# Kernel optimization log

Measured on AMD Instinct MI355X. Metric: run time of the kernel, lower is better.

The kernel has to match this reference:

```python
import jax, jax.numpy as jnp
import numpy as np

D_MODEL = 1024
N_HEADS = 16
HEAD_DIM = D_MODEL // N_HEADS


def setup_inputs() -> dict:
    key = jax.random.key(0)
    k_x, k_qkv, k_out = jax.random.split(key, 3)
    B, T = 4, 2048
    x = jax.random.normal(k_x, (B, T, D_MODEL), dtype=jnp.float32)
    # Linear(bias=False): y = x @ W, with W stored as [in, out]
    W_qkv = jax.random.normal(k_qkv, (D_MODEL, 3 * D_MODEL), dtype=jnp.float32) * (D_MODEL ** -0.5)
    W_out = jax.random.normal(k_out, (D_MODEL, D_MODEL), dtype=jnp.float32) * (D_MODEL ** -0.5)
    return {"x": x, "W_qkv": W_qkv, "W_out": W_out}


def reference(x, W_qkv, W_out):
    B, T, C = x.shape
    H, Dh = N_HEADS, HEAD_DIM
    scale = 1.0 / jnp.sqrt(jnp.asarray(Dh, dtype=x.dtype))

    qkv = x @ W_qkv  # [B,T,3C]
    q, k, v = jnp.split(qkv, 3, axis=-1)

    def split_heads(t):
        return t.reshape(B, T, H, Dh).transpose(0, 2, 1, 3)  # [B,H,T,Dh]

    q, k, v = split_heads(q), split_heads(k), split_heads(v)

    scores = jnp.einsum('bhqd,bhkd->bhqk', q, k) * scale  # [B,H,T,T]
    causal = jnp.tril(jnp.ones((T, T), dtype=bool))
    scores = jnp.where(causal, scores, jnp.asarray(-jnp.inf, dtype=scores.dtype))
    attn = jax.nn.softmax(scores, axis=-1)
    # dropout p=0.0 -> identity
    out = jnp.einsum('bhqk,bhkd->bhqd', attn, v)  # [B,H,T,Dh]
    out = out.transpose(0, 2, 1, 3).reshape(B, T, C)
    return out @ W_out
```

## Files before the change

### kernel.cpp

```cpp
#include <hip/hip_runtime.h>
#include <stdint.h>

typedef unsigned short u16;
typedef float f32x4 __attribute__((ext_vector_type(4)));
typedef short s16x8 __attribute__((ext_vector_type(8)));

#define SEQ 2048
#define DM 1024
#define NH 16
#define HD 64
#define BATCH 4
#define ROWS (BATCH*SEQ)

__device__ __forceinline__ u16 f32_bf16(float f) {
  union { float f; uint32_t u; } c; c.f = f;
  uint32_t u = c.u;
  return (u16)((u + 0x7fffu + ((u >> 16) & 1u)) >> 16);
}
__device__ __forceinline__ u16 f32_bf16_trunc(float f) {
  union { float f; uint32_t u; } c; c.f = f;
  return (u16)(c.u >> 16);
}

#define GLOAD_LDS16(g, l) __builtin_amdgcn_global_load_lds( \
    (__attribute__((address_space(1))) void*)(g),           \
    (__attribute__((address_space(3))) void*)(l), 16, 0, 0)

__global__ __launch_bounds__(256) void cast_bf16_k(const float* __restrict__ in,
                                                   u16* __restrict__ out, int n4) {
  int i = blockIdx.x * 256 + threadIdx.x;
  if (i >= n4) return;
  float4 v = ((const float4*)in)[i];
  ushort4 o;
  o.x = f32_bf16(v.x); o.y = f32_bf16(v.y); o.z = f32_bf16(v.z); o.w = f32_bf16(v.w);
  ((ushort4*)out)[i] = o;
}

__global__ __launch_bounds__(256) void cast_transpose_k(const float* __restrict__ in,
                                                        u16* __restrict__ out, int R, int C) {
  __shared__ float tile[32][33];
  int c0 = blockIdx.x * 32, r0 = blockIdx.y * 32;
  int t = threadIdx.x;
  int lr = t >> 3, lc = (t & 7) * 4;
  float4 v = *(const float4*)(in + (size_t)(r0 + lr) * C + c0 + lc);
  tile[lr][lc] = v.x; tile[lr][lc + 1] = v.y; tile[lr][lc + 2] = v.z; tile[lr][lc + 3] = v.w;
  __syncthreads();
  ushort4 o;
  o.x = f32_bf16(tile[lc + 0][lr]);
  o.y = f32_bf16(tile[lc + 1][lr]);
  o.z = f32_bf16(tile[lc + 2][lr]);
  o.w = f32_bf16(tile[lc + 3][lr]);
  *(ushort4*)(out + (size_t)(c0 + lr) * R + r0 + lc) = o;
}

#define QSCALE 0.18033688011112042f


__device__ __forceinline__ f32x4 mfma16(s16x8 a, s16x8 b, f32x4 c) {
  return __builtin_amdgcn_mfma_f32_16x16x32_bf16(a, b, c, 0, 0, 0);
}

template<int STG, int ENDVM, int LAST>
__device__ __forceinline__ void tile_step(
    const u16* lAc, const u16* lBc,
    const u16* lAn, const u16* lBn,
    u16* lAs, u16* lBs,
    const u16* gA0, const u16* gA1, const u16* gB0, const u16* gB1,
    int d0, int d1, int aoff, int boff,
    s16x8 (&fa)[4], s16x8 (&fb)[4],
    s16x8 (&na)[4], s16x8 (&nb)[4],
    f32x4 (&acc)[8][4])
{
  __builtin_amdgcn_s_barrier();
  __builtin_amdgcn_sched_barrier(0);
  s16x8 f1[4];
#pragma unroll
  for (int mi = 0; mi < 4; ++mi) f1[mi] = *(const s16x8*)&lAc[aoff + 2048 + mi * 512];
  if (STG) { GLOAD_LDS16(gA0, lAs + d0); GLOAD_LDS16(gA1, lAs + d1); }
  asm volatile("s_waitcnt lgkmcnt(4)" ::: "memory");
  __builtin_amdgcn_sched_barrier(0);
  __builtin_amdgcn_s_setprio(1);
#pragma unroll
  for (int mi = 0; mi < 4; ++mi)
#pragma unroll
    for (int ni = 0; ni < 4; ++ni)
      acc[mi][ni] = mfma16(fa[mi], fb[ni], acc[mi][ni]);
  __builtin_amdgcn_s_setprio(0);
  __builtin_amdgcn_sched_barrier(0);
  if (STG) { GLOAD_LDS16(gB0, lBs + d0); GLOAD_LDS16(gB1, lBs + d1); }
  if (ENDVM == 8)      asm volatile("s_waitcnt vmcnt(8)" ::: "memory");
  else if (ENDVM == 4) asm volatile("s_waitcnt vmcnt(4)" ::: "memory");
  else if (ENDVM == 0) asm volatile("s_waitcnt vmcnt(0)" ::: "memory");
  __builtin_amdgcn_s_barrier();
  __builtin_amdgcn_sched_barrier(0);
  if (!LAST) {
#pragma unroll
    for (int ni = 0; ni < 4; ++ni) nb[ni] = *(const s16x8*)&lBn[boff + ni * 512];
#pragma unroll
    for (int mi = 0; mi < 4; ++mi) na[mi] = *(const s16x8*)&lAn[aoff + mi * 512];
    asm volatile("s_waitcnt lgkmcnt(8)" ::: "memory");
  } else {
    asm volatile("s_waitcnt lgkmcnt(0)" ::: "memory");
  }
  __builtin_amdgcn_sched_barrier(0);
  __builtin_amdgcn_s_setprio(1);
#pragma unroll
  for (int mi = 0; mi < 4; ++mi)
#pragma unroll
    for (int ni = 0; ni < 4; ++ni)
      acc[4 + mi][ni] = mfma16(f1[mi], fb[ni], acc[4 + mi][ni]);
  __builtin_amdgcn_s_setprio(0);
  __builtin_amdgcn_sched_barrier(0);
}

__global__ __launch_bounds__(512, 2) void qkv_gemm(
    const u16* __restrict__ A, const u16* __restrict__ Bt,
    u16* __restrict__ Qo, u16* __restrict__ Ko, u16* __restrict__ Vo)
{
  __shared__ u16 lA[4][8192];
  __shared__ u16 lB[4][8192];
  int t = threadIdx.x;

  int flat = blockIdx.y * 12 + blockIdx.x;
  int xcd = flat & 7, idx = flat >> 3;
  int by = (xcd >> 1) * 8 + idx / 6;
  int bx = (xcd & 1) * 6 + idx % 6;
  int m0 = by * 256, n0 = bx * 256;

  int lane = t & 63, w = t >> 6;
  int m16 = lane & 15, quad = lane >> 4;
  int wm = w >> 2, wn = w & 3;

  int r0 = t >> 2;
  int scol = ((t & 3) ^ ((t >> 3) & 3)) * 8;
  const u16* Ag0 = A  + (size_t)(m0 + r0) * DM + scol;
  const u16* Ag1 = A  + (size_t)(m0 + 128 + r0) * DM + scol;
  const u16* Bg0 = Bt + (size_t)(n0 + r0) * DM + scol;
  const u16* Bg1 = Bt + (size_t)(n0 + 128 + r0) * DM + scol;
  int d0 = t * 8, d1 = 4096 + t * 8;

  int ka = (quad ^ ((m16 >> 1) & 3)) * 8;
  int aoff = (wm * 128 + m16) * 32 + ka;
  int boff = (wn * 64 + m16) * 32 + ka;

  f32x4 acc[8][4];
#pragma unroll
  for (int mi = 0; mi < 8; ++mi)
#pragma unroll
    for (int ni = 0; ni < 4; ++ni)
#pragma unroll
      for (int r = 0; r < 4; ++r) acc[mi][ni][r] = 0.f;

#pragma unroll
  for (int kt = 0; kt < 3; ++kt) {
    GLOAD_LDS16(Ag0 + kt * 32, lA[kt] + d0);
    GLOAD_LDS16(Ag1 + kt * 32, lA[kt] + d1);
    GLOAD_LDS16(Bg0 + kt * 32, lB[kt] + d0);
    GLOAD_LDS16(Bg1 + kt * 32, lB[kt] + d1);
  }
  asm volatile("s_waitcnt vmcnt(8)" ::: "memory");
  __builtin_amdgcn_s_barrier();
  __builtin_amdgcn_sched_barrier(0);

  s16x8 fa0[4], fb0[4], fa1[4], fb1[4];
#pragma unroll
  for (int ni = 0; ni < 4; ++ni) fb0[ni] = *(const s16x8*)&lB[0][boff + ni * 512];
#pragma unroll
  for (int mi = 0; mi < 4; ++mi) fa0[mi] = *(const s16x8*)&lA[0][aoff + mi * 512];

  for (int it = 0; it < 14; ++it) {
    int T = 2 * it;
    tile_step<1, 8, 0>(lA[T & 3], lB[T & 3], lA[(T + 1) & 3], lB[(T + 1) & 3],
                       lA[(T + 3) & 3], lB[(T + 3) & 3],
                       Ag0 + (T + 3) * 32, Ag1 + (T + 3) * 32,
                       Bg0 + (T + 3) * 32, Bg1 + (T + 3) * 32,
                       d0, d1, aoff, boff, fa0, fb0, fa1, fb1, acc);
    tile_step<1, 8, 0>(lA[(T + 1) & 3], lB[(T + 1) & 3], lA[(T + 2) & 3], lB[(T + 2) & 3],
                       lA[(T + 4) & 3], lB[(T + 4) & 3],
                       Ag0 + (T + 4) * 32, Ag1 + (T + 4) * 32,
                       Bg0 + (T + 4) * 32, Bg1 + (T + 4) * 32,
                       d0, d1, aoff, boff, fa1, fb1, fa0, fb0, acc);
  }
  tile_step<1, 8, 0>(lA[0], lB[0], lA[1], lB[1], lA[3], lB[3],
                     Ag0 + 31 * 32, Ag1 + 31 * 32, Bg0 + 31 * 32, Bg1 + 31 * 32,
                     d0, d1, aoff, boff, fa0, fb0, fa1, fb1, acc);
  tile_step<0, 4, 0>(lA[1], lB[1], lA[2], lB[2], lA[0], lB[0],
                     Ag0, Ag1, Bg0, Bg1, d0, d1, aoff, boff, fa1, fb1, fa0, fb0, acc);
  tile_step<0, 0, 0>(lA[2], lB[2], lA[3], lB[3], lA[0], lB[0],
                     Ag0, Ag1, Bg0, Bg1, d0, d1, aoff, boff, fa0, fb0, fa1, fb1, acc);
  tile_step<0, -1, 1>(lA[3], lB[3], lA[0], lB[0], lA[0], lB[0],
                      Ag0, Ag1, Bg0, Bg1, d0, d1, aoff, boff, fa1, fb1, fa0, fb0, acc);

#pragma unroll
  for (int mi = 0; mi < 8; ++mi) {
    int gr = m0 + wm * 128 + mi * 16 + quad * 4;
    int b = gr >> 11, tt = gr & 2047;
#pragma unroll
    for (int ni = 0; ni < 4; ++ni) {
      int gc = n0 + wn * 64 + ni * 16 + m16;
      int sec = gc >> 10, rem = gc & 1023, h = rem >> 6, d = rem & 63;
      if (sec == 0) {
#pragma unroll
        for (int r = 0; r < 4; ++r)
          Qo[(((size_t)b * NH + h) * SEQ + tt + r) * HD + d] = f32_bf16(acc[mi][ni][r] * QSCALE);
      } else if (sec == 1) {
#pragma unroll
        for (int r = 0; r < 4; ++r)
          Ko[(((size_t)b * NH + h) * SEQ + tt + r) * HD + d] = f32_bf16(acc[mi][ni][r]);
      } else {
        ushort4 o;
        o.x = f32_bf16(acc[mi][ni][0]); o.y = f32_bf16(acc[mi][ni][1]);
        o.z = f32_bf16(acc[mi][ni][2]); o.w = f32_bf16(acc[mi][ni][3]);
        *(ushort4*)&Vo[(((size_t)b * NH + h) * HD + d) * SEQ + tt] = o;
      }
    }
  }
}

template<int EPI>
__global__ __launch_bounds__(256) void gemm_bt(
    const u16* __restrict__ A, const u16* __restrict__ Bt,
    float* __restrict__ Cf, u16* __restrict__ Qo, u16* __restrict__ Ko, u16* __restrict__ Vo,
    int M, int N, int K)
{
  __shared__ u16 As[128 * 32];
  __shared__ u16 Bs[128 * 32];
  int t = threadIdx.x;
  int m0 = blockIdx.y * 128, n0 = blockIdx.x * 128;

  int srow = t >> 2, scol8 = (t & 3) * 8;
  const u16* Ag0 = A  + (size_t)(m0 + srow) * K + scol8;
  const u16* Ag1 = A  + (size_t)(m0 + 64 + srow) * K + scol8;
  const u16* Bg0 = Bt + (size_t)(n0 + srow) * K + scol8;
  const u16* Bg1 = Bt + (size_t)(n0 + 64 + srow) * K + scol8;
  u16* Al0 = As + t * 8;  u16* Al1 = As + 2048 + t * 8;
  u16* Bl0 = Bs + t * 8;  u16* Bl1 = Bs + 2048 + t * 8;

  int lane = t & 63, w = t >> 6;
  int m16 = lane & 15, quad = lane >> 4;
  int wr = (w >> 1) * 64, wc = (w & 1) * 64;

  f32x4 acc[4][4];
#pragma unroll
  for (int mi = 0; mi < 4; ++mi)
#pragma unroll
    for (int ni = 0; ni < 4; ++ni)
#pragma unroll
      for (int r = 0; r < 4; ++r) acc[mi][ni][r] = 0.f;

  for (int k0 = 0; k0 < K; k0 += 32) {
    __syncthreads();
    GLOAD_LDS16(Ag0 + k0, Al0);
    GLOAD_LDS16(Ag1 + k0, Al1);
    GLOAD_LDS16(Bg0 + k0, Bl0);
    GLOAD_LDS16(Bg1 + k0, Bl1);
    __syncthreads();
    s16x8 af[4], bf[4];
#pragma unroll
    for (int mi = 0; mi < 4; ++mi)
      af[mi] = *(const s16x8*)(As + (wr + mi * 16 + m16) * 32 + quad * 8);
#pragma unroll
    for (int ni = 0; ni < 4; ++ni)
      bf[ni] = *(const s16x8*)(Bs + (wc + ni * 16 + m16) * 32 + quad * 8);
#pragma unroll
    for (int mi = 0; mi < 4; ++mi)
#pragma unroll
      for (int ni = 0; ni < 4; ++ni)
        acc[mi][ni] = __builtin_amdgcn_mfma_f32_16x16x32_bf16(af[mi], bf[ni], acc[mi][ni], 0, 0, 0);
  }

  if (EPI == 0) {
#pragma unroll
    for (int mi = 0; mi < 4; ++mi) {
      int gr = m0 + wr + mi * 16 + quad * 4;
#pragma unroll
      for (int ni = 0; ni < 4; ++ni) {
        int gc = n0 + wc + ni * 16 + m16;
#pragma unroll
        for (int r = 0; r < 4; ++r)
          Cf[(size_t)(gr + r) * N + gc] = acc[mi][ni][r];
      }
    }
  } else {
#pragma unroll
    for (int mi = 0; mi < 4; ++mi) {
      int gr = m0 + wr + mi * 16 + quad * 4;
      int b = gr >> 11, tt = gr & 2047;
#pragma unroll
      for (int ni = 0; ni < 4; ++ni) {
        int gc = n0 + wc + ni * 16 + m16;
        int sec = gc >> 10, rem = gc & 1023, h = rem >> 6, d = rem & 63;
        if (sec == 0) {
#pragma unroll
          for (int r = 0; r < 4; ++r)
            Qo[(((size_t)b * NH + h) * SEQ + tt + r) * HD + d] = f32_bf16(acc[mi][ni][r] * QSCALE);
        } else if (sec == 1) {
#pragma unroll
          for (int r = 0; r < 4; ++r)
            Ko[(((size_t)b * NH + h) * SEQ + tt + r) * HD + d] = f32_bf16(acc[mi][ni][r]);
        } else {
          ushort4 o;
          o.x = f32_bf16(acc[mi][ni][0]); o.y = f32_bf16(acc[mi][ni][1]);
          o.z = f32_bf16(acc[mi][ni][2]); o.w = f32_bf16(acc[mi][ni][3]);
          *(ushort4*)&Vo[(((size_t)b * NH + h) * HD + d) * SEQ + tt] = o;
        }
      }
    }
  }
}

__global__ __launch_bounds__(256) void attn_k(
    const u16* __restrict__ Q, const u16* __restrict__ K,
    const u16* __restrict__ Vt_g,
    u16* __restrict__ O)
{
  __shared__ u16 Ks[64][72];
  __shared__ u16 Vt[64][72];
  __shared__ u16 Ps[4][32][72];
  int flat = blockIdx.y * 8 + blockIdx.x;
  int xcd = flat & 7, pos = flat >> 3;
  int bh = xcd * 8 + (pos >> 3);
  int xb = pos & 7;
  int t = threadIdx.x, w = t >> 6, lane = t & 63;
  int m16 = lane & 15, quad = lane >> 4;
  int b = bh >> 4, h = bh & 15;

  int srow = t >> 2, sc = (t & 3) * 16;
  const u16* Kg0 = K    + ((size_t)bh * SEQ + srow) * HD  + sc;
  const u16* Vg0 = Vt_g + ((size_t)bh * HD  + srow) * SEQ + sc;

  for (int half = 0; half < 2; ++half) {
    int qt = half ? (15 - xb) : xb;
    int q0 = qt * 128;

    const u16* QbA = Q + ((size_t)bh * SEQ + q0 + w * 32 + m16) * HD + quad * 8;
    s16x8 qA0 = *(const s16x8*)QbA;
    s16x8 qA1 = *(const s16x8*)(QbA + 32);
    s16x8 qB0 = *(const s16x8*)(QbA + 16 * HD);
    s16x8 qB1 = *(const s16x8*)(QbA + 16 * HD + 32);

    f32x4 accA[4], accB[4];
    float lA = 0.f, lB = 0.f;
#pragma unroll
    for (int ni = 0; ni < 4; ++ni)
#pragma unroll
      for (int r = 0; r < 4; ++r) { accA[ni][r] = 0.f; accB[ni][r] = 0.f; }

    int ktmax = 2 * qt + 1;
    for (int kt = 0; kt <= ktmax; ++kt) {
      uint4 kv0 = *(const uint4*)(Kg0 + (size_t)kt * 64 * HD);
      uint4 kv1 = *(const uint4*)(Kg0 + (size_t)kt * 64 * HD + 8);
      uint4 vv0 = *(const uint4*)(Vg0 + kt * 64);
      uint4 vv1 = *(const uint4*)(Vg0 + kt * 64 + 8);
      __syncthreads();
      *(uint4*)&Ks[srow][sc]     = kv0;
      *(uint4*)&Ks[srow][sc + 8] = kv1;
      *(uint4*)&Vt[srow][sc]     = vv0;
      *(uint4*)&Vt[srow][sc + 8] = vv1;
      __syncthreads();

      f32x4 sA[4], sB[4];
#pragma unroll
      for (int ni = 0; ni < 4; ++ni)
#pragma unroll
        for (int r = 0; r < 4; ++r) { sA[ni][r] = 0.f; sB[ni][r] = 0.f; }
#pragma unroll
      for (int ni = 0; ni < 4; ++ni) {
        s16x8 kf0 = *(const s16x8*)&Ks[ni * 16 + m16][quad * 8];
        s16x8 kf1 = *(const s16x8*)&Ks[ni * 16 + m16][32 + quad * 8];
        sA[ni] = mfma16(kf0, qA0, sA[ni]);
        sA[ni] = mfma16(kf1, qA1, sA[ni]);
        sB[ni] = mfma16(kf0, qB0, sB[ni]);
        sB[ni] = mfma16(kf1, qB1, sB[ni]);
      }
      if (kt >= 2 * qt) {
        int qga = q0 + w * 32 + m16;
#pragma unroll
        for (int ni = 0; ni < 4; ++ni) {
          int kb = kt * 64 + ni * 16 + quad * 4;
#pragma unroll
          for (int r = 0; r < 4; ++r) {
            if (kb + r > qga)      sA[ni][r] = -1e30f;
            if (kb + r > qga + 16) sB[ni][r] = -1e30f;
          }
        }
      }

#pragma unroll
      for (int ni = 0; ni < 4; ++ni) {
        ushort4 oA, oB;
#pragma unroll
        for (int r = 0; r < 4; ++r) {
          float pA = __builtin_amdgcn_exp2f(sA[ni][r]);
          float pB = __builtin_amdgcn_exp2f(sB[ni][r]);
          lA += pA; lB += pB;
          ((u16*)&oA)[r] = f32_bf16_trunc(pA);
          ((u16*)&oB)[r] = f32_bf16_trunc(pB);
        }
        *(ushort4*)&Ps[w][m16][ni * 16 + quad * 4]      = oA;
        *(ushort4*)&Ps[w][16 + m16][ni * 16 + quad * 4] = oB;
      }

#pragma unroll
      for (int ks = 0; ks < 2; ++ks) {
        s16x8 pA = *(const s16x8*)&Ps[w][m16][ks * 32 + quad * 8];
        s16x8 pB = *(const s16x8*)&Ps[w][16 + m16][ks * 32 + quad * 8];
#pragma unroll
        for (int ni = 0; ni < 4; ++ni) {
          s16x8 vf = *(const s16x8*)&Vt[ni * 16 + m16][ks * 32 + quad * 8];
          accA[ni] = mfma16(pA, vf, accA[ni]);
          accB[ni] = mfma16(pB, vf, accB[ni]);
        }
      }
    }

    lA += __shfl_xor(lA, 16, 64);
    lA += __shfl_xor(lA, 32, 64);
    lB += __shfl_xor(lB, 16, 64);
    lB += __shfl_xor(lB, 32, 64);

#pragma unroll
    for (int r = 0; r < 4; ++r) {
      int src = (lane & 48) | (quad * 4 + r);
      float la = __shfl(lA, src, 64);
      float lb = __shfl(lB, src, 64);
      float ia = 1.f / la, ib = 1.f / lb;
      int qa = q0 + w * 32 + quad * 4 + r;
      size_t baseA = ((size_t)(b * SEQ + qa)) * DM + h * HD;
      size_t baseB = baseA + (size_t)16 * DM;
#pragma unroll
      for (int ni = 0; ni < 4; ++ni) {
        O[baseA + ni * 16 + m16] = f32_bf16(accA[ni][r] * ia);
        O[baseB + ni * 16 + m16] = f32_bf16(accB[ni][r] * ib);
      }
    }
  }
}

extern "C" void kernel_launch(void* const* d_in, const int* in_sizes, int n_in,
                              void* d_out, int out_size, void* d_ws, size_t ws_size,
                              hipStream_t stream) {
  const float* x    = (const float*)d_in[0];
  const float* Wqkv = (const float*)d_in[1];
  const float* Wout = (const float*)d_in[2];
  float* out = (float*)d_out;

  u16* ws = (u16*)d_ws;
  size_t off = 0;
  u16* x_bf   = ws + off; off += (size_t)ROWS * DM;
  u16* wqkv_t = ws + off; off += (size_t)(3 * DM) * DM;
  u16* wout_t = ws + off; off += (size_t)DM * DM;
  u16* Qb     = ws + off; off += (size_t)BATCH * NH * SEQ * HD;
  u16* Kb     = ws + off; off += (size_t)BATCH * NH * SEQ * HD;
  u16* Vb     = ws + off; off += (size_t)BATCH * NH * SEQ * HD;
  u16* AO     = ws + off; off += (size_t)ROWS * DM;

  cast_bf16_k<<<(ROWS * DM / 4 + 255) / 256, 256, 0, stream>>>(x, x_bf, ROWS * DM / 4);
  cast_transpose_k<<<dim3(3 * DM / 32, DM / 32), 256, 0, stream>>>(Wqkv, wqkv_t, DM, 3 * DM);
  cast_transpose_k<<<dim3(DM / 32, DM / 32), 256, 0, stream>>>(Wout, wout_t, DM, DM);
  qkv_gemm<<<dim3(12, 32), 512, 0, stream>>>(x_bf, wqkv_t, Qb, Kb, Vb);
  attn_k<<<dim3(8, BATCH * NH), 256, 0, stream>>>(Qb, Kb, Vb, AO);
  gemm_bt<0><<<dim3(DM / 128, ROWS / 128), 256, 0, stream>>>(
      AO, wout_t, out, nullptr, nullptr, nullptr, ROWS, DM, DM);
}
```

Before: 255.7 us.

## Restructure QKV GEMM pipeline into double-buffered 64-wide K tiles

Replaces the four-stage 32-wide K ring buffer with cross-step fragment prefetch by a two-buffer scheme where each step covers 64 K elements in four sub-phases. Fragments are loaded and consumed within the same sub-phase, with barriers around each load and a full lgkmcnt wait. The goal is simpler scheduling with fewer register-held fragments and larger loads per stage. The cost is less LDS-read/MFMA overlap and more barriers per K tile, so latency may be exposed.

```diff
diff --git a/kernel.cpp b/kernel.cpp
--- a/kernel.cpp
+++ b/kernel.cpp
@@ -60,65 +60,90 @@
   return __builtin_amdgcn_mfma_f32_16x16x32_bf16(a, b, c, 0, 0, 0);
 }
 
-template<int STG, int ENDVM, int LAST>
-__device__ __forceinline__ void tile_step(
-    const u16* lAc, const u16* lBc,
-    const u16* lAn, const u16* lBn,
-    u16* lAs, u16* lBs,
+template<int STG, int VM2, int VM4>
+__device__ __forceinline__ void qkv_tile(
+    const u16* Ac, const u16* Bc,
+    u16* Asd, u16* Bsd,
     const u16* gA0, const u16* gA1, const u16* gB0, const u16* gB1,
     int d0, int d1, int aoff, int boff,
-    s16x8 (&fa)[4], s16x8 (&fb)[4],
-    s16x8 (&na)[4], s16x8 (&nb)[4],
     f32x4 (&acc)[8][4])
 {
-  __builtin_amdgcn_s_barrier();
-  __builtin_amdgcn_sched_barrier(0);
-  s16x8 f1[4];
-#pragma unroll
-  for (int mi = 0; mi < 4; ++mi) f1[mi] = *(const s16x8*)&lAc[aoff + 2048 + mi * 512];
-  if (STG) { GLOAD_LDS16(gA0, lAs + d0); GLOAD_LDS16(gA1, lAs + d1); }
-  asm volatile("s_waitcnt lgkmcnt(4)" ::: "memory");
+  s16x8 bfr[4], af[4];
+#pragma unroll
+  for (int ni = 0; ni < 4; ++ni) bfr[ni] = *(const s16x8*)&Bc[boff + ni * 512];
+#pragma unroll
+  for (int mi = 0; mi < 4; ++mi) af[mi] = *(const s16x8*)&Ac[aoff + mi * 512];
+  if (STG) { GLOAD_LDS16(gA0, Asd + d0); GLOAD_LDS16(gA1, Asd + d1); }
+  __builtin_amdgcn_s_barrier();
+  asm volatile("s_waitcnt lgkmcnt(0)" ::: "memory");
   __builtin_amdgcn_sched_barrier(0);
   __builtin_amdgcn_s_setprio(1);
 #pragma unroll
   for (int mi = 0; mi < 4; ++mi)
 #pragma unroll
     for (int ni = 0; ni < 4; ++ni)
-      acc[mi][ni] = mfma16(fa[mi], fb[ni], acc[mi][ni]);
+      acc[mi][ni] = mfma16(af[mi], bfr[ni], acc[mi][ni]);
   __builtin_amdgcn_s_setprio(0);
   __builtin_amdgcn_sched_barrier(0);
-  if (STG) { GLOAD_LDS16(gB0, lBs + d0); GLOAD_LDS16(gB1, lBs + d1); }
-  if (ENDVM == 8)      asm volatile("s_waitcnt vmcnt(8)" ::: "memory");
-  else if (ENDVM == 4) asm volatile("s_waitcnt vmcnt(4)" ::: "memory");
-  else if (ENDVM == 0) asm volatile("s_waitcnt vmcnt(0)" ::: "memory");
-  __builtin_amdgcn_s_barrier();
-  __builtin_amdgcn_sched_barrier(0);
-  if (!LAST) {
-#pragma unroll
-    for (int ni = 0; ni < 4; ++ni) nb[ni] = *(const s16x8*)&lBn[boff + ni * 512];
-#pragma unroll
-    for (int mi = 0; mi < 4; ++mi) na[mi] = *(const s16x8*)&lAn[aoff + mi * 512];
-    asm volatile("s_waitcnt lgkmcnt(8)" ::: "memory");
-  } else {
-    asm volatile("s_waitcnt lgkmcnt(0)" ::: "memory");
-  }
+  __builtin_amdgcn_s_barrier();
+#pragma unroll
+  for (int mi = 0; mi < 4; ++mi) af[mi] = *(const s16x8*)&Ac[aoff + 2048 + mi * 512];
+  if (STG) { GLOAD_LDS16(gB0, Bsd + d0); GLOAD_LDS16(gB1, Bsd + d1); }
+  __builtin_amdgcn_s_barrier();
+  asm volatile("s_waitcnt lgkmcnt(0)" ::: "memory");
   __builtin_amdgcn_sched_barrier(0);
   __builtin_amdgcn_s_setprio(1);
 #pragma unroll
   for (int mi = 0; mi < 4; ++mi)
 #pragma unroll
     for (int ni = 0; ni < 4; ++ni)
-      acc[4 + mi][ni] = mfma16(f1[mi], fb[ni], acc[4 + mi][ni]);
+      acc[4 + mi][ni] = mfma16(af[mi], bfr[ni], acc[4 + mi][ni]);
   __builtin_amdgcn_s_setprio(0);
   __builtin_amdgcn_sched_barrier(0);
+  if (VM2 == 4)      asm volatile("s_waitcnt vmcnt(4)" ::: "memory");
+  else if (VM2 == 0) asm volatile("s_waitcnt vmcnt(0)" ::: "memory");
+  __builtin_amdgcn_s_barrier();
+#pragma unroll
+  for (int ni = 0; ni < 4; ++ni) bfr[ni] = *(const s16x8*)&Bc[8192 + boff + ni * 512];
+#pragma unroll
+  for (int mi = 0; mi < 4; ++mi) af[mi] = *(const s16x8*)&Ac[8192 + aoff + mi * 512];
+  if (STG) { GLOAD_LDS16(gA0 + 32, Asd + 8192 + d0); GLOAD_LDS16(gA1 + 32, Asd + 8192 + d1); }
+  __builtin_amdgcn_s_barrier();
+  asm volatile("s_waitcnt lgkmcnt(0)" ::: "memory");
+  __builtin_amdgcn_sched_barrier(0);
+  __builtin_amdgcn_s_setprio(1);
+#pragma unroll
+  for (int mi = 0; mi < 4; ++mi)
+#pragma unroll
+    for (int ni = 0; ni < 4; ++ni)
+      acc[mi][ni] = mfma16(af[mi], bfr[ni], acc[mi][ni]);
+  __builtin_amdgcn_s_setprio(0);
+  __builtin_amdgcn_sched_barrier(0);
+  __builtin_amdgcn_s_barrier();
+#pragma unroll
+  for (int mi = 0; mi < 4; ++mi) af[mi] = *(const s16x8*)&Ac[8192 + aoff + 2048 + mi * 512];
+  if (STG) { GLOAD_LDS16(gB0 + 32, Bsd + 8192 + d0); GLOAD_LDS16(gB1 + 32, Bsd + 8192 + d1); }
+  __builtin_amdgcn_s_barrier();
+  asm volatile("s_waitcnt lgkmcnt(0)" ::: "memory");
+  __builtin_amdgcn_sched_barrier(0);
+  __builtin_amdgcn_s_setprio(1);
+#pragma unroll
+  for (int mi = 0; mi < 4; ++mi)
+#pragma unroll
+    for (int ni = 0; ni < 4; ++ni)
+      acc[4 + mi][ni] = mfma16(af[mi], bfr[ni], acc[4 + mi][ni]);
+  __builtin_amdgcn_s_setprio(0);
+  __builtin_amdgcn_sched_barrier(0);
+  if (VM4 == 4) asm volatile("s_waitcnt vmcnt(4)" ::: "memory");
+  __builtin_amdgcn_s_barrier();
 }
 
 __global__ __launch_bounds__(512, 2) void qkv_gemm(
     const u16* __restrict__ A, const u16* __restrict__ Bt,
     u16* __restrict__ Qo, u16* __restrict__ Ko, u16* __restrict__ Vo)
 {
-  __shared__ u16 lA[4][8192];
-  __shared__ u16 lB[4][8192];
+  __shared__ u16 lA[2][16384];
+  __shared__ u16 lB[2][16384];
   int t = threadIdx.x;
 
   int flat = blockIdx.y * 12 + blockIdx.x;
@@ -151,45 +176,27 @@
 #pragma unroll
       for (int r = 0; r < 4; ++r) acc[mi][ni][r] = 0.f;
 
-#pragma unroll
-  for (int kt = 0; kt < 3; ++kt) {
-    GLOAD_LDS16(Ag0 + kt * 32, lA[kt] + d0);
-    GLOAD_LDS16(Ag1 + kt * 32, lA[kt] + d1);
-    GLOAD_LDS16(Bg0 + kt * 32, lB[kt] + d0);
-    GLOAD_LDS16(Bg1 + kt * 32, lB[kt] + d1);
+  GLOAD_LDS16(Ag0, lA[0] + d0);
+  GLOAD_LDS16(Ag1, lA[0] + d1);
+  GLOAD_LDS16(Bg0, lB[0] + d0);
+  GLOAD_LDS16(Bg1, lB[0] + d1);
+  GLOAD_LDS16(Ag0 + 32, lA[0] + 8192 + d0);
+  GLOAD_LDS16(Ag1 + 32, lA[0] + 8192 + d1);
+  GLOAD_LDS16(Bg0 + 32, lB[0] + 8192 + d0);
+  GLOAD_LDS16(Bg1 + 32, lB[0] + 8192 + d1);
+  asm volatile("s_waitcnt vmcnt(4)" ::: "memory");
+  __builtin_amdgcn_s_barrier();
+  __builtin_amdgcn_sched_barrier(0);
+
+  for (int T = 0; T < 15; ++T) {
+    int db = T & 1;
+    qkv_tile<1, 4, 4>(lA[db], lB[db], lA[db ^ 1], lB[db ^ 1],
+                      Ag0 + (T + 1) * 64, Ag1 + (T + 1) * 64,
+                      Bg0 + (T + 1) * 64, Bg1 + (T + 1) * 64,
+                      d0, d1, aoff, boff, acc);
   }
-  asm volatile("s_waitcnt vmcnt(8)" ::: "memory");
-  __builtin_amdgcn_s_barrier();
-  __builtin_amdgcn_sched_barrier(0);
-
-  s16x8 fa0[4], fb0[4], fa1[4], fb1[4];
-#pragma unroll
-  for (int ni = 0; ni < 4; ++ni) fb0[ni] = *(const s16x8*)&lB[0][boff + ni * 512];
-#pragma unroll
-  for (int mi = 0; mi < 4; ++mi) fa0[mi] = *(const s16x8*)&lA[0][aoff + mi * 512];
-
-  for (int it = 0; it < 14; ++it) {
-    int T = 2 * it;
-    tile_step<1, 8, 0>(lA[T & 3], lB[T & 3], lA[(T + 1) & 3], lB[(T + 1) & 3],
-                       lA[(T + 3) & 3], lB[(T + 3) & 3],
-                       Ag0 + (T + 3) * 32, Ag1 + (T + 3) * 32,
-                       Bg0 + (T + 3) * 32, Bg1 + (T + 3) * 32,
-                       d0, d1, aoff, boff, fa0, fb0, fa1, fb1, acc);
-    tile_step<1, 8, 0>(lA[(T + 1) & 3], lB[(T + 1) & 3], lA[(T + 2) & 3], lB[(T + 2) & 3],
-                       lA[(T + 4) & 3], lB[(T + 4) & 3],
-                       Ag0 + (T + 4) * 32, Ag1 + (T + 4) * 32,
-                       Bg0 + (T + 4) * 32, Bg1 + (T + 4) * 32,
-                       d0, d1, aoff, boff, fa1, fb1, fa0, fb0, acc);
-  }
-  tile_step<1, 8, 0>(lA[0], lB[0], lA[1], lB[1], lA[3], lB[3],
-                     Ag0 + 31 * 32, Ag1 + 31 * 32, Bg0 + 31 * 32, Bg1 + 31 * 32,
-                     d0, d1, aoff, boff, fa0, fb0, fa1, fb1, acc);
-  tile_step<0, 4, 0>(lA[1], lB[1], lA[2], lB[2], lA[0], lB[0],
-                     Ag0, Ag1, Bg0, Bg1, d0, d1, aoff, boff, fa1, fb1, fa0, fb0, acc);
-  tile_step<0, 0, 0>(lA[2], lB[2], lA[3], lB[3], lA[0], lB[0],
-                     Ag0, Ag1, Bg0, Bg1, d0, d1, aoff, boff, fa0, fb0, fa1, fb1, acc);
-  tile_step<0, -1, 1>(lA[3], lB[3], lA[0], lB[0], lA[0], lB[0],
-                      Ag0, Ag1, Bg0, Bg1, d0, d1, aoff, boff, fa1, fb1, fa0, fb0, acc);
+  qkv_tile<0, 0, -1>(lA[1], lB[1], lA[0], lB[0],
+                     Ag0, Ag1, Bg0, Bg1, d0, d1, aoff, boff, acc);
 
 #pragma unroll
   for (int mi = 0; mi < 8; ++mi) {
```

After: 262.8 us. 2.8% more time.

## Retile QKV GEMM to 128x384 blocks and swizzle attention LDS layouts

Applied to the files above, without the earlier changes.

The QKV projection GEMM moves from 256x256 tiles on a 12x32 grid to 128x384 tiles on an 8x64 grid, which doubles the block count and changes each wave's fragment shape to 2x6 MFMA tiles. The XCD-aware block remapping and the LDS staging are updated to match. Separately, the attention kernel drops its padded 72-wide K, V and P shared buffers in favour of split low/high 32-column buffers with XOR swizzling, meant to avoid bank conflicts without the padding. The GEMM retile shifts the balance between wave count and per-tile reuse, and the swizzled indexing adds address arithmetic.

```diff
diff --git a/kernel.cpp b/kernel.cpp
--- a/kernel.cpp
+++ b/kernel.cpp
@@ -65,29 +65,33 @@
     const u16* lAc, const u16* lBc,
     const u16* lAn, const u16* lBn,
     u16* lAs, u16* lBs,
-    const u16* gA0, const u16* gA1, const u16* gB0, const u16* gB1,
-    int d0, int d1, int aoff, int boff,
-    s16x8 (&fa)[4], s16x8 (&fb)[4],
-    s16x8 (&na)[4], s16x8 (&nb)[4],
-    f32x4 (&acc)[8][4])
+    const u16* gA, const u16* gB0, const u16* gB1, const u16* gB2,
+    int d0, int aoff, int boff,
+    s16x8 (&fa)[2], s16x8 (&fb)[6],
+    s16x8 (&na)[2], s16x8 (&nb)[6],
+    f32x4 (&acc)[4][6])
 {
   __builtin_amdgcn_s_barrier();
   __builtin_amdgcn_sched_barrier(0);
-  s16x8 f1[4];
-#pragma unroll
-  for (int mi = 0; mi < 4; ++mi) f1[mi] = *(const s16x8*)&lAc[aoff + 2048 + mi * 512];
-  if (STG) { GLOAD_LDS16(gA0, lAs + d0); GLOAD_LDS16(gA1, lAs + d1); }
-  asm volatile("s_waitcnt lgkmcnt(4)" ::: "memory");
+  s16x8 f1[2];
+#pragma unroll
+  for (int mi = 0; mi < 2; ++mi) f1[mi] = *(const s16x8*)&lAc[aoff + 1024 + mi * 512];
+  if (STG) { GLOAD_LDS16(gA, lAs + d0); }
+  asm volatile("s_waitcnt lgkmcnt(2)" ::: "memory");
   __builtin_amdgcn_sched_barrier(0);
   __builtin_amdgcn_s_setprio(1);
 #pragma unroll
-  for (int mi = 0; mi < 4; ++mi)
-#pragma unroll
-    for (int ni = 0; ni < 4; ++ni)
+  for (int mi = 0; mi < 2; ++mi)
+#pragma unroll
+    for (int ni = 0; ni < 6; ++ni)
       acc[mi][ni] = mfma16(fa[mi], fb[ni], acc[mi][ni]);
   __builtin_amdgcn_s_setprio(0);
   __builtin_amdgcn_sched_barrier(0);
-  if (STG) { GLOAD_LDS16(gB0, lBs + d0); GLOAD_LDS16(gB1, lBs + d1); }
+  if (STG) {
+    GLOAD_LDS16(gB0, lBs + d0);
+    GLOAD_LDS16(gB1, lBs + 4096 + d0);
+    GLOAD_LDS16(gB2, lBs + 8192 + d0);
+  }
   if (ENDVM == 8)      asm volatile("s_waitcnt vmcnt(8)" ::: "memory");
   else if (ENDVM == 4) asm volatile("s_waitcnt vmcnt(4)" ::: "memory");
   else if (ENDVM == 0) asm volatile("s_waitcnt vmcnt(0)" ::: "memory");
@@ -95,9 +99,9 @@
   __builtin_amdgcn_sched_barrier(0);
   if (!LAST) {
 #pragma unroll
-    for (int ni = 0; ni < 4; ++ni) nb[ni] = *(const s16x8*)&lBn[boff + ni * 512];
-#pragma unroll
-    for (int mi = 0; mi < 4; ++mi) na[mi] = *(const s16x8*)&lAn[aoff + mi * 512];
+    for (int ni = 0; ni < 6; ++ni) nb[ni] = *(const s16x8*)&lBn[boff + ni * 512];
+#pragma unroll
+    for (int mi = 0; mi < 2; ++mi) na[mi] = *(const s16x8*)&lAn[aoff + mi * 512];
     asm volatile("s_waitcnt lgkmcnt(8)" ::: "memory");
   } else {
     asm volatile("s_waitcnt lgkmcnt(0)" ::: "memory");
@@ -105,10 +109,10 @@
   __builtin_amdgcn_sched_barrier(0);
   __builtin_amdgcn_s_setprio(1);
 #pragma unroll
-  for (int mi = 0; mi < 4; ++mi)
-#pragma unroll
-    for (int ni = 0; ni < 4; ++ni)
-      acc[4 + mi][ni] = mfma16(f1[mi], fb[ni], acc[4 + mi][ni]);
+  for (int mi = 0; mi < 2; ++mi)
+#pragma unroll
+    for (int ni = 0; ni < 6; ++ni)
+      acc[2 + mi][ni] = mfma16(f1[mi], fb[ni], acc[2 + mi][ni]);
   __builtin_amdgcn_s_setprio(0);
   __builtin_amdgcn_sched_barrier(0);
 }
@@ -117,15 +121,15 @@
     const u16* __restrict__ A, const u16* __restrict__ Bt,
     u16* __restrict__ Qo, u16* __restrict__ Ko, u16* __restrict__ Vo)
 {
-  __shared__ u16 lA[4][8192];
-  __shared__ u16 lB[4][8192];
+  __shared__ u16 lA[4][4096];
+  __shared__ u16 lB[4][12288];
   int t = threadIdx.x;
 
-  int flat = blockIdx.y * 12 + blockIdx.x;
+  int flat = blockIdx.y * 8 + blockIdx.x;
   int xcd = flat & 7, idx = flat >> 3;
-  int by = (xcd >> 1) * 8 + idx / 6;
-  int bx = (xcd & 1) * 6 + idx % 6;
-  int m0 = by * 256, n0 = bx * 256;
+  int by = (xcd >> 1) * 16 + (idx >> 2);
+  int bx = (xcd & 1) * 4 + (idx & 3);
+  int m0 = by * 128, n0 = bx * 384;
 
   int lane = t & 63, w = t >> 6;
   int m16 = lane & 15, quad = lane >> 4;
@@ -133,71 +137,72 @@
 
   int r0 = t >> 2;
   int scol = ((t & 3) ^ ((t >> 3) & 3)) * 8;
-  const u16* Ag0 = A  + (size_t)(m0 + r0) * DM + scol;
-  const u16* Ag1 = A  + (size_t)(m0 + 128 + r0) * DM + scol;
+  const u16* Ag  = A  + (size_t)(m0 + r0) * DM + scol;
   const u16* Bg0 = Bt + (size_t)(n0 + r0) * DM + scol;
   const u16* Bg1 = Bt + (size_t)(n0 + 128 + r0) * DM + scol;
-  int d0 = t * 8, d1 = 4096 + t * 8;
+  const u16* Bg2 = Bt + (size_t)(n0 + 256 + r0) * DM + scol;
+  int d0 = t * 8;
 
   int ka = (quad ^ ((m16 >> 1) & 3)) * 8;
-  int aoff = (wm * 128 + m16) * 32 + ka;
-  int boff = (wn * 64 + m16) * 32 + ka;
-
-  f32x4 acc[8][4];
-#pragma unroll
-  for (int mi = 0; mi < 8; ++mi)
-#pragma unroll
-    for (int ni = 0; ni < 4; ++ni)
+  int aoff = (wm * 64 + m16) * 32 + ka;
+  int boff = (wn * 96 + m16) * 32 + ka;
+
+  f32x4 acc[4][6];
+#pragma unroll
+  for (int mi = 0; mi < 4; ++mi)
+#pragma unroll
+    for (int ni = 0; ni < 6; ++ni)
 #pragma unroll
       for (int r = 0; r < 4; ++r) acc[mi][ni][r] = 0.f;
 
 #pragma unroll
   for (int kt = 0; kt < 3; ++kt) {
-    GLOAD_LDS16(Ag0 + kt * 32, lA[kt] + d0);
-    GLOAD_LDS16(Ag1 + kt * 32, lA[kt] + d1);
+    GLOAD_LDS16(Ag + kt * 32, lA[kt] + d0);
     GLOAD_LDS16(Bg0 + kt * 32, lB[kt] + d0);
-    GLOAD_LDS16(Bg1 + kt * 32, lB[kt] + d1);
+    GLOAD_LDS16(Bg1 + kt * 32, lB[kt] + 4096 + d0);
+    GLOAD_LDS16(Bg2 + kt * 32, lB[kt] + 8192 + d0);
   }
   asm volatile("s_waitcnt vmcnt(8)" ::: "memory");
   __builtin_amdgcn_s_barrier();
   __builtin_amdgcn_sched_barrier(0);
 
-  s16x8 fa0[4], fb0[4], fa1[4], fb1[4];
-#pragma unroll
-  for (int ni = 0; ni < 4; ++ni) fb0[ni] = *(const s16x8*)&lB[0][boff + ni * 512];
-#pragma unroll
-  for (int mi = 0; mi < 4; ++mi) fa0[mi] = *(const s16x8*)&lA[0][aoff + mi * 512];
+  s16x8 fa0[2], fa1[2];
+  s16x8 fb0[6], fb1[6];
+#pragma unroll
+  for (int ni = 0; ni < 6; ++ni) fb0[ni] = *(const s16x8*)&lB[0][boff + ni * 512];
+#pragma unroll
+  for (int mi = 0; mi < 2; ++mi) fa0[mi] = *(const s16x8*)&lA[0][aoff + mi * 512];
 
   for (int it = 0; it < 14; ++it) {
     int T = 2 * it;
     tile_step<1, 8, 0>(lA[T & 3], lB[T & 3], lA[(T + 1) & 3], lB[(T + 1) & 3],
                        lA[(T + 3) & 3], lB[(T + 3) & 3],
-                       Ag0 + (T + 3) * 32, Ag1 + (T + 3) * 32,
-                       Bg0 + (T + 3) * 32, Bg1 + (T + 3) * 32,
-                       d0, d1, aoff, boff, fa0, fb0, fa1, fb1, acc);
+                       Ag + (T + 3) * 32,
+                       Bg0 + (T + 3) * 32, Bg1 + (T + 3) * 32, Bg2 + (T + 3) * 32,
+                       d0, aoff, boff, fa0, fb0, fa1, fb1, acc);
     tile_step<1, 8, 0>(lA[(T + 1) & 3], lB[(T + 1) & 3], lA[(T + 2) & 3], lB[(T + 2) & 3],
                        lA[(T + 4) & 3], lB[(T + 4) & 3],
-                       Ag0 + (T + 4) * 32, Ag1 + (T + 4) * 32,
-                       Bg0 + (T + 4) * 32, Bg1 + (T + 4) * 32,
-                       d0, d1, aoff, boff, fa1, fb1, fa0, fb0, acc);
+                       Ag + (T + 4) * 32,
+                       Bg0 + (T + 4) * 32, Bg1 + (T + 4) * 32, Bg2 + (T + 4) * 32,
+                       d0, aoff, boff, fa1, fb1, fa0, fb0, acc);
   }
   tile_step<1, 8, 0>(lA[0], lB[0], lA[1], lB[1], lA[3], lB[3],
-                     Ag0 + 31 * 32, Ag1 + 31 * 32, Bg0 + 31 * 32, Bg1 + 31 * 32,
-                     d0, d1, aoff, boff, fa0, fb0, fa1, fb1, acc);
+                     Ag + 31 * 32, Bg0 + 31 * 32, Bg1 + 31 * 32, Bg2 + 31 * 32,
+                     d0, aoff, boff, fa0, fb0, fa1, fb1, acc);
   tile_step<0, 4, 0>(lA[1], lB[1], lA[2], lB[2], lA[0], lB[0],
-                     Ag0, Ag1, Bg0, Bg1, d0, d1, aoff, boff, fa1, fb1, fa0, fb0, acc);
+                     Ag, Bg0, Bg1, Bg2, d0, aoff, boff, fa1, fb1, fa0, fb0, acc);
   tile_step<0, 0, 0>(lA[2], lB[2], lA[3], lB[3], lA[0], lB[0],
-                     Ag0, Ag1, Bg0, Bg1, d0, d1, aoff, boff, fa0, fb0, fa1, fb1, acc);
+                     Ag, Bg0, Bg1, Bg2, d0, aoff, boff, fa0, fb0, fa1, fb1, acc);
   tile_step<0, -1, 1>(lA[3], lB[3], lA[0], lB[0], lA[0], lB[0],
-                      Ag0, Ag1, Bg0, Bg1, d0, d1, aoff, boff, fa1, fb1, fa0, fb0, acc);
-
-#pragma unroll
-  for (int mi = 0; mi < 8; ++mi) {
-    int gr = m0 + wm * 128 + mi * 16 + quad * 4;
+                      Ag, Bg0, Bg1, Bg2, d0, aoff, boff, fa1, fb1, fa0, fb0, acc);
+
+#pragma unroll
+  for (int mi = 0; mi < 4; ++mi) {
+    int gr = m0 + wm * 64 + mi * 16 + quad * 4;
     int b = gr >> 11, tt = gr & 2047;
 #pragma unroll
-    for (int ni = 0; ni < 4; ++ni) {
-      int gc = n0 + wn * 64 + ni * 16 + m16;
+    for (int ni = 0; ni < 6; ++ni) {
+      int gc = n0 + wn * 96 + ni * 16 + m16;
       int sec = gc >> 10, rem = gc & 1023, h = rem >> 6, d = rem & 63;
       if (sec == 0) {
 #pragma unroll
@@ -314,9 +319,9 @@
     const u16* __restrict__ Vt_g,
     u16* __restrict__ O)
 {
-  __shared__ u16 Ks[64][72];
-  __shared__ u16 Vt[64][72];
-  __shared__ u16 Ps[4][32][72];
+  __shared__ u16 KsL[64][32], KsH[64][32];
+  __shared__ u16 VtL[64][32], VtH[64][32];
+  __shared__ u16 PsL[4][32][32], PsH[4][32][32];
   int flat = blockIdx.y * 8 + blockIdx.x;
   int xcd = flat & 7, pos = flat >> 3;
   int bh = xcd * 8 + (pos >> 3);
@@ -329,6 +334,15 @@
   const u16* Kg0 = K    + ((size_t)bh * SEQ + srow) * HD  + sc;
   const u16* Vg0 = Vt_g + ((size_t)bh * HD  + srow) * SEQ + sc;
 
+  int rsw = (srow >> 1) & 3;
+  int lc = (sc & 31) >> 3;
+  int c0 = lc ^ rsw;
+  u16* KsD = (sc >= 32 ? &KsH[0][0] : &KsL[0][0]) + srow * 32;
+  u16* VtD = (sc >= 32 ? &VtH[0][0] : &VtL[0][0]) + srow * 32;
+
+  int kka = (quad ^ ((m16 >> 1) & 3)) * 8;
+  int psw = (m16 >> 1) & 3;
+
   for (int half = 0; half < 2; ++half) {
     int qt = half ? (15 - xb) : xb;
     int q0 = qt * 128;
@@ -353,10 +367,10 @@
       uint4 vv0 = *(const uint4*)(Vg0 + kt * 64);
       uint4 vv1 = *(const uint4*)(Vg0 + kt * 64 + 8);
       __syncthreads();
-      *(uint4*)&Ks[srow][sc]     = kv0;
-      *(uint4*)&Ks[srow][sc + 8] = kv1;
-      *(uint4*)&Vt[srow][sc]     = vv0;
-      *(uint4*)&Vt[srow][sc + 8] = vv1;
+      *(uint4*)(KsD + c0 * 8)       = kv0;
+      *(uint4*)(KsD + (c0 ^ 1) * 8) = kv1;
+      *(uint4*)(VtD + c0 * 8)       = vv0;
+      *(uint4*)(VtD + (c0 ^ 1) * 8) = vv1;
       __syncthreads();
 
       f32x4 sA[4], sB[4];
@@ -366,8 +380,9 @@
         for (int r = 0; r < 4; ++r) { sA[ni][r] = 0.f; sB[ni][r] = 0.f; }
 #pragma unroll
       for (int ni = 0; ni < 4; ++ni) {
-        s16x8 kf0 = *(const s16x8*)&Ks[ni * 16 + m16][quad * 8];
-        s16x8 kf1 = *(const s16x8*)&Ks[ni * 16 + m16][32 + quad * 8];
+        int krow = (ni * 16 + m16) * 32 + kka;
+        s16x8 kf0 = *(const s16x8*)(&KsL[0][0] + krow);
+        s16x8 kf1 = *(const s16x8*)(&KsH[0][0] + krow);
         sA[ni] = mfma16(kf0, qA0, sA[ni]);
         sA[ni] = mfma16(kf1, qA1, sA[ni]);
         sB[ni] = mfma16(kf0, qB0, sB[ni]);
@@ -397,17 +412,21 @@
           ((u16*)&oA)[r] = f32_bf16_trunc(pA);
           ((u16*)&oB)[r] = f32_bf16_trunc(pB);
         }
-        *(ushort4*)&Ps[w][m16][ni * 16 + quad * 4]      = oA;
-        *(ushort4*)&Ps[w][16 + m16][ni * 16 + quad * 4] = oB;
+        u16* pd = (ni >= 2 ? &PsH[w][0][0] : &PsL[w][0][0]);
+        int cs = (((ni & 1) * 2 + (quad >> 1)) ^ psw) * 8 + (quad & 1) * 4;
+        *(ushort4*)(pd + m16 * 32 + cs)        = oA;
+        *(ushort4*)(pd + (16 + m16) * 32 + cs) = oB;
       }
 
 #pragma unroll
       for (int ks = 0; ks < 2; ++ks) {
-        s16x8 pA = *(const s16x8*)&Ps[w][m16][ks * 32 + quad * 8];
-        s16x8 pB = *(const s16x8*)&Ps[w][16 + m16][ks * 32 + quad * 8];
+        const u16* ps = ks ? &PsH[w][0][0] : &PsL[w][0][0];
+        const u16* vb = ks ? &VtH[0][0] : &VtL[0][0];
+        s16x8 pA = *(const s16x8*)(ps + m16 * 32 + kka);
+        s16x8 pB = *(const s16x8*)(ps + (16 + m16) * 32 + kka);
 #pragma unroll
         for (int ni = 0; ni < 4; ++ni) {
-          s16x8 vf = *(const s16x8*)&Vt[ni * 16 + m16][ks * 32 + quad * 8];
+          s16x8 vf = *(const s16x8*)(vb + (ni * 16 + m16) * 32 + kka);
           accA[ni] = mfma16(pA, vf, accA[ni]);
           accB[ni] = mfma16(pB, vf, accB[ni]);
         }
@@ -458,7 +477,7 @@
   cast_bf16_k<<<(ROWS * DM / 4 + 255) / 256, 256, 0, stream>>>(x, x_bf, ROWS * DM / 4);
   cast_transpose_k<<<dim3(3 * DM / 32, DM / 32), 256, 0, stream>>>(Wqkv, wqkv_t, DM, 3 * DM);
   cast_transpose_k<<<dim3(DM / 32, DM / 32), 256, 0, stream>>>(Wout, wout_t, DM, DM);
-  qkv_gemm<<<dim3(12, 32), 512, 0, stream>>>(x_bf, wqkv_t, Qb, Kb, Vb);
+  qkv_gemm<<<dim3(8, 64), 512, 0, stream>>>(x_bf, wqkv_t, Qb, Kb, Vb);
   attn_k<<<dim3(8, BATCH * NH), 256, 0, stream>>>(Qb, Kb, Vb, AO);
   gemm_bt<0><<<dim3(DM / 128, ROWS / 128), 256, 0, stream>>>(
       AO, wout_t, out, nullptr, nullptr, nullptr, ROWS, DM, DM);
```

New measurement: 257.8 us. No clear change (+0.8%).
